# Kernel optimization log

Measured on AMD Instinct MI355X. Metric: run time of the kernel, lower is better.

## Reference

```python
import jax, jax.numpy as jnp
import numpy as np

GROUPS = 32  # from analyze_enhance_linear_ops(4096, 4096, 0.05): smallest divisor g with 1/g <= 0.05


def setup_inputs() -> dict:
    key = jax.random.key(0)
    k1, k2, k3, k4, k5 = jax.random.split(key, 5)
    B, S, D_in, D_out = 4, 2048, 4096, 4096
    ig = D_out // GROUPS  # 128
    x = jax.random.normal(k1, (B, S, D_in), dtype=jnp.float32)
    W = jax.random.normal(k2, (D_out, D_in), dtype=jnp.float32) * 0.02
    b = jax.random.normal(k3, (D_out,), dtype=jnp.float32) * 0.02
    Wg = jax.random.normal(k4, (GROUPS, ig, ig), dtype=jnp.float32) * 0.02
    bg = jax.random.normal(k5, (GROUPS, ig), dtype=jnp.float32) * 0.02
    return {"x": x, "W": W, "b": b, "Wg": Wg, "bg": bg}


def reference(x, W, b, Wg, bg):
    # original_linear: dense GEMM, torch Linear layout W[out, in]
    y = jnp.einsum('bsi,oi->bso', x, W) + b            # [B, S, D_out]
    # GroupedLinear: block-diagonal transform over groups of size out_group
    B, S, D = y.shape
    G, og, ig = Wg.shape
    yg = y.reshape(B, S, G, ig)                        # split into groups
    out = jnp.einsum('bsgi,goi->bsgo', yg, Wg) + bg    # per-group small GEMM + bias
    return out.reshape(B, S, D)                        # cat along feature dim
```

## Files before the change

### kernel.cpp

```cpp
#include <hip/hip_runtime.h>
#include <hip/hip_bf16.h>
#include <stdint.h>

typedef float f32x4 __attribute__((ext_vector_type(4)));
typedef float f32x16 __attribute__((ext_vector_type(16)));
typedef short s16x8 __attribute__((ext_vector_type(8)));
typedef unsigned int u32x2 __attribute__((ext_vector_type(2)));
typedef unsigned int u32x4 __attribute__((ext_vector_type(4)));

#define MDIM 8192
#define NDIM 4096
#define KDIM 4096
#define NKT  64

__device__ __forceinline__ unsigned pkbf(float lo, float hi) {
  unsigned short l = __builtin_bit_cast(unsigned short, __float2bfloat16(lo));
  unsigned short h = __builtin_bit_cast(unsigned short, __float2bfloat16(hi));
  return ((unsigned)h << 16) | (unsigned)l;
}

__device__ __forceinline__ void gload16(const void* g, void* l) {
  __builtin_amdgcn_global_load_lds((const __attribute__((address_space(1))) int*)g,
                                   (__attribute__((address_space(3))) int*)l, 16, 0, 0);
}

__global__ __launch_bounds__(256) void conv_tile(
    const float* __restrict__ X, const float* __restrict__ W,
    s16x8* __restrict__ wsA, s16x8* __restrict__ wsB) {
  __shared__ char lds[32768];
  const int b = blockIdx.x;
  const int tid = threadIdx.x;
  const float* src;
  s16x8* dst;
  int bi;
  if (b < 32 * NKT) { src = X; dst = wsA; bi = b; }
  else              { src = W; dst = wsB; bi = b - 32 * NKT; }
  const int rt = bi >> 6;
  const int kt = bi & 63;
  const int fr = tid >> 4;
  const int c4 = (tid & 15) * 4;
  const int h = c4 >> 5;
  const int ks2 = (c4 >> 4) & 1;
  const int lh = (c4 & 15) >> 3;
  const int e2 = (c4 & 7) * 2;
  #pragma unroll
  for (int f = 0; f < 16; ++f) {
    const int row = f * 16 + fr;
    f32x4 v = *(const f32x4*)(src + ((size_t)rt * 256 + row) * KDIM + kt * 64 + c4);
    u32x2 p = { pkbf(v[0], v[1]), pkbf(v[2], v[3]) };
    const int frag = (h * 2 + ks2) * 8 + (f >> 1);
    const int lane = lh * 32 + (f & 1) * 16 + fr;
    *(u32x2*)(lds + frag * 1024 + lane * 16 + e2) = p;
  }
  __syncthreads();
  const size_t ob = (size_t)bi * 2048;
  #pragma unroll
  for (int i = 0; i < 8; ++i)
    dst[ob + i * 256 + tid] = *(const s16x8*)(lds + (i * 256 + tid) * 16);
}

__global__ __launch_bounds__(512, 2) void gemm256(
    const s16x8* __restrict__ wsA, const s16x8* __restrict__ wsB,
    const float* __restrict__ bias, const float* __restrict__ Wg,
    const float* __restrict__ bg, float* __restrict__ out) {
  extern __shared__ char smem[];
  const int tid = threadIdx.x;
  const int lane = tid & 63;
  const int wid = tid >> 6;
  const int wr = wid >> 2;
  const int wc = wid & 3;
  const int c32 = lane & 31;
  const int q5 = lane >> 5;

  const int bid = blockIdx.x;
  const int swz = (bid & 7) * 64 + (bid >> 3);
  const int bm = swz >> 4;
  const int bn = swz & 15;

  const size_t aBase = (size_t)bm * NKT * 2048;
  const size_t bBase = (size_t)bn * NKT * 2048;

  auto stage = [&](int kt, int db, int isB, int h) {
    const s16x8* s = (isB ? wsB + bBase : wsA + aBase)
                     + (size_t)kt * 2048 + h * 1024 + wid * 128 + lane;
    char* d = smem + isB * 65536 + db * 32768 + h * 16384 + wid * 2048;
    gload16(s, d);
    gload16(s + 64, d + 1024);
  };

  const char* aRd = smem + wr * 4096 + lane * 16;
  const char* bRd = smem + 65536 + wc * 2048 + lane * 16;

  f32x16 acc[4][2];
  #pragma unroll
  for (int m = 0; m < 4; ++m)
    #pragma unroll
    for (int n = 0; n < 2; ++n) acc[m][n] = (f32x16)0.0f;

  s16x8 af[4], bfr[2];

#define SP(DB, H, KS2, SKT, SDB, SOP, SH, DOVM)                                \
  {                                                                            \
    stage(SKT, SDB, SOP, SH);                                                  \
    _Pragma("unroll")                                                          \
    for (int n = 0; n < 2; ++n)                                                \
      bfr[n] = *(const s16x8*)(bRd + (DB)*32768 + (H)*16384 + (KS2)*8192 + n * 1024); \
    _Pragma("unroll")                                                          \
    for (int m = 0; m < 4; ++m)                                                \
      af[m] = *(const s16x8*)(aRd + (DB)*32768 + (H)*16384 + (KS2)*8192 + m * 1024);  \
    if (DOVM) asm volatile("s_waitcnt vmcnt(4)" ::: "memory");                 \
    __builtin_amdgcn_s_barrier();                                              \
    asm volatile("s_waitcnt lgkmcnt(0)" ::: "memory");                         \
    __builtin_amdgcn_s_setprio(1);                                             \
    _Pragma("unroll")                                                          \
    for (int m = 0; m < 4; ++m) {                                              \
      _Pragma("unroll")                                                        \
      for (int n = 0; n < 2; ++n)                                              \
        acc[m][n] = __builtin_amdgcn_mfma_f32_32x32x16_bf16(                   \
            af[m], bfr[n], acc[m][n], 0, 0, 0);                                \
    }                                                                          \
    __builtin_amdgcn_s_setprio(0);                                             \
  }

  stage(0, 0, 0, 0); stage(0, 0, 1, 0);
  stage(0, 0, 0, 1); stage(0, 0, 1, 1);
  stage(1, 1, 0, 0); stage(1, 1, 1, 0);
  asm volatile("s_waitcnt vmcnt(4)" ::: "memory");
  __builtin_amdgcn_s_barrier();

  #pragma clang loop unroll(disable)
  for (int it = 0; it < 32; ++it) {
    const int u0 = 2 * it;
    const int k1 = u0 + 1;
    const int k2 = (u0 + 2 < NKT) ? u0 + 2 : NKT - 1;
    const int k3 = (u0 + 3 < NKT) ? u0 + 3 : NKT - 1;
    SP(0, 0, 0, k1, 1, 0, 1, 0)
    SP(0, 0, 1, k1, 1, 1, 1, 0)
    SP(0, 1, 0, k2, 0, 0, 0, 0)
    SP(0, 1, 1, k2, 0, 1, 0, 1)
    SP(1, 0, 0, k2, 0, 0, 1, 0)
    SP(1, 0, 1, k2, 0, 1, 1, 0)
    SP(1, 1, 0, k3, 1, 0, 0, 0)
    SP(1, 1, 1, k3, 1, 1, 0, 1)
  }
#undef SP

  asm volatile("s_waitcnt vmcnt(0)" ::: "memory");
  asm volatile("s_waitcnt lgkmcnt(0)" ::: "memory");
  __builtin_amdgcn_s_barrier();

  float bv[2];
  #pragma unroll
  for (int n = 0; n < 2; ++n) bv[n] = bias[bn * 256 + wc * 64 + n * 32 + c32];

  {
    const int e2 = (c32 & 7) * 2;
    const int lh = (c32 >> 3) & 1;
    #pragma unroll
    for (int m = 0; m < 4; ++m) {
      const int Mf = wr * 4 + m;
      #pragma unroll
      for (int n = 0; n < 2; ++n) {
        const int Kc = wc * 4 + n * 2 + (c32 >> 4);
        char* base = smem + (Mf * 16 + Kc) * 1024 + lh * 512 + e2;
        #pragma unroll
        for (int r = 0; r < 16; ++r) {
          const int rl = (r & 3) + 8 * (r >> 2) + 4 * q5;
          const float y = acc[m][n][r] + bv[n];
          *(unsigned short*)(base + rl * 16) =
              __builtin_bit_cast(unsigned short, __float2bfloat16(y));
        }
      }
    }
  }
  asm volatile("s_waitcnt lgkmcnt(0)" ::: "memory");
  __builtin_amdgcn_s_barrier();

  const int g = bn * 2 + (wc >> 1);
  const float* wgb = Wg + (size_t)g * 16384;
  f32x16 acc2[4][2];
  #pragma unroll
  for (int m = 0; m < 4; ++m)
    #pragma unroll
    for (int n = 0; n < 2; ++n) acc2[m][n] = (f32x16)0.0f;

  #pragma unroll
  for (int ks = 0; ks < 8; ++ks) {
    const int Kc = (wc >> 1) * 8 + ks;
    s16x8 af2[4];
    #pragma unroll
    for (int m = 0; m < 4; ++m)
      af2[m] = *(const s16x8*)(smem + ((wr * 4 + m) * 16 + Kc) * 1024 + lane * 16);
    #pragma unroll
    for (int n = 0; n < 2; ++n) {
      const int ocl = (wc & 1) * 64 + n * 32 + c32;
      const float* wp = wgb + ocl * 128 + ks * 16 + q5 * 8;
      f32x4 w0 = *(const f32x4*)wp;
      f32x4 w1 = *(const f32x4*)(wp + 4);
      u32x4 pw = { pkbf(w0[0], w0[1]), pkbf(w0[2], w0[3]),
                   pkbf(w1[0], w1[1]), pkbf(w1[2], w1[3]) };
      const s16x8 bfw = __builtin_bit_cast(s16x8, pw);
      #pragma unroll
      for (int m = 0; m < 4; ++m)
        acc2[m][n] = __builtin_amdgcn_mfma_f32_32x32x16_bf16(af2[m], bfw, acc2[m][n], 0, 0, 0);
    }
  }

  float bgv[2];
  #pragma unroll
  for (int n = 0; n < 2; ++n) bgv[n] = bg[bn * 256 + wc * 64 + n * 32 + c32];

  #pragma unroll
  for (int m = 0; m < 4; ++m) {
    #pragma unroll
    for (int n = 0; n < 2; ++n) {
      const int col = bn * 256 + wc * 64 + n * 32 + c32;
      #pragma unroll
      for (int r = 0; r < 16; ++r) {
        const size_t row = (size_t)bm * 256 + wr * 128 + m * 32
                         + (r & 3) + 8 * (r >> 2) + 4 * q5;
        out[row * NDIM + col] = acc2[m][n][r] + bgv[n];
      }
    }
  }
}

extern "C" void kernel_launch(void* const* d_in, const int* in_sizes, int n_in,
                              void* d_out, int out_size, void* d_ws, size_t ws_size,
                              hipStream_t stream) {
  const float* X    = (const float*)d_in[0];
  const float* W    = (const float*)d_in[1];
  const float* bias = (const float*)d_in[2];
  const float* Wg   = (const float*)d_in[3];
  const float* bg   = (const float*)d_in[4];
  float* out = (float*)d_out;

  s16x8* wsA = (s16x8*)d_ws;
  s16x8* wsB = wsA + ((size_t)MDIM * KDIM / 8);

  hipFuncSetAttribute(reinterpret_cast<const void*>(gemm256),
                      hipFuncAttributeMaxDynamicSharedMemorySize, 131072);

  conv_tile<<<dim3(3072), dim3(256), 0, stream>>>(X, W, wsA, wsB);
  gemm256<<<dim3(512), dim3(512), 131072, stream>>>(wsA, wsB, bias, Wg, bg, out);
}
```

Before: 310.3 us.

## Load B fragments directly from global into registers, stage only A in LDS

The B operand is no longer staged through shared memory. Each wave loads its B fragments straight from global memory into registers, double-buffered across k-steps, while A keeps a 4-slot LDS ring. This halves LDS traffic and async-copy bookkeeping, but each B tile is now fetched separately by every wave row instead of once per block. That relies on cache hits, and exposed global latency may stall the MFMAs.

```diff
diff --git a/kernel.cpp b/kernel.cpp
--- a/kernel.cpp
+++ b/kernel.cpp
@@ -77,19 +77,17 @@
   const int bm = swz >> 4;
   const int bn = swz & 15;
 
-  const size_t aBase = (size_t)bm * NKT * 2048;
-  const size_t bBase = (size_t)bn * NKT * 2048;
-
-  auto stage = [&](int kt, int db, int isB, int h) {
-    const s16x8* s = (isB ? wsB + bBase : wsA + aBase)
-                     + (size_t)kt * 2048 + h * 1024 + wid * 128 + lane;
-    char* d = smem + isB * 65536 + db * 32768 + h * 16384 + wid * 2048;
+  const char* wsAb = (const char*)wsA + ((size_t)bm << 21);
+  const char* wsBb = (const char*)wsB + ((size_t)bn << 21);
+
+  auto stageA = [&](int t, int slot) {
+    const char* s = wsAb + ((size_t)t << 14) + (wid << 11) + (lane << 4);
+    char* d = smem + (slot << 14) + (wid << 11);
     gload16(s, d);
-    gload16(s + 64, d + 1024);
+    gload16(s + 1024, d + 1024);
   };
 
-  const char* aRd = smem + wr * 4096 + lane * 16;
-  const char* bRd = smem + 65536 + wc * 2048 + lane * 16;
+  const char* aRd = smem + (wr << 12) + (lane << 4);
 
   f32x16 acc[4][2];
   #pragma unroll
@@ -97,53 +95,58 @@
     #pragma unroll
     for (int n = 0; n < 2; ++n) acc[m][n] = (f32x16)0.0f;
 
-  s16x8 af[4], bfr[2];
-
-#define SP(DB, H, KS2, SKT, SDB, SOP, SH, DOVM)                                \
-  {                                                                            \
-    stage(SKT, SDB, SOP, SH);                                                  \
-    _Pragma("unroll")                                                          \
-    for (int n = 0; n < 2; ++n)                                                \
-      bfr[n] = *(const s16x8*)(bRd + (DB)*32768 + (H)*16384 + (KS2)*8192 + n * 1024); \
-    _Pragma("unroll")                                                          \
-    for (int m = 0; m < 4; ++m)                                                \
-      af[m] = *(const s16x8*)(aRd + (DB)*32768 + (H)*16384 + (KS2)*8192 + m * 1024);  \
-    if (DOVM) asm volatile("s_waitcnt vmcnt(4)" ::: "memory");                 \
-    __builtin_amdgcn_s_barrier();                                              \
-    asm volatile("s_waitcnt lgkmcnt(0)" ::: "memory");                         \
-    __builtin_amdgcn_s_setprio(1);                                             \
-    _Pragma("unroll")                                                          \
-    for (int m = 0; m < 4; ++m) {                                              \
-      _Pragma("unroll")                                                        \
-      for (int n = 0; n < 2; ++n)                                              \
-        acc[m][n] = __builtin_amdgcn_mfma_f32_32x32x16_bf16(                   \
-            af[m], bfr[n], acc[m][n], 0, 0, 0);                                \
-    }                                                                          \
-    __builtin_amdgcn_s_setprio(0);                                             \
-  }
-
-  stage(0, 0, 0, 0); stage(0, 0, 1, 0);
-  stage(0, 0, 0, 1); stage(0, 0, 1, 1);
-  stage(1, 1, 0, 0); stage(1, 1, 1, 0);
-  asm volatile("s_waitcnt vmcnt(4)" ::: "memory");
+  s16x8 af[4], bE[2], bO[2];
+
+  const char* bAddr = wsBb + ((wc * 2) << 10) + (lane << 4);
+
+  stageA(0, 0);
+  stageA(1, 1);
+  #pragma unroll
+  for (int n = 0; n < 2; ++n)
+    bE[n] = *(const s16x8*)(bAddr + ((size_t)0 << 13) + (n << 10));
+  asm volatile("s_waitcnt vmcnt(2)" ::: "memory");
   __builtin_amdgcn_s_barrier();
 
   #pragma clang loop unroll(disable)
-  for (int it = 0; it < 32; ++it) {
-    const int u0 = 2 * it;
-    const int k1 = u0 + 1;
-    const int k2 = (u0 + 2 < NKT) ? u0 + 2 : NKT - 1;
-    const int k3 = (u0 + 3 < NKT) ? u0 + 3 : NKT - 1;
-    SP(0, 0, 0, k1, 1, 0, 1, 0)
-    SP(0, 0, 1, k1, 1, 1, 1, 0)
-    SP(0, 1, 0, k2, 0, 0, 0, 0)
-    SP(0, 1, 1, k2, 0, 1, 0, 1)
-    SP(1, 0, 0, k2, 0, 0, 1, 0)
-    SP(1, 0, 1, k2, 0, 1, 1, 0)
-    SP(1, 1, 0, k3, 1, 0, 0, 0)
-    SP(1, 1, 1, k3, 1, 1, 0, 1)
-  }
-#undef SP
+  for (int t = 0; t < 128; ++t) {
+    const int tn = (t + 2 < 128) ? t + 2 : 127;
+    const size_t k1 = 2 * t + 1;
+    const size_t k2 = (2 * t + 2 < 256) ? 2 * t + 2 : 255;
+    const int slot = t & 3;
+    stageA(tn, (t + 2) & 3);
+    #pragma unroll
+    for (int n = 0; n < 2; ++n)
+      bO[n] = *(const s16x8*)(bAddr + (k1 << 13) + (n << 10));
+    #pragma unroll
+    for (int m = 0; m < 4; ++m)
+      af[m] = *(const s16x8*)(aRd + (slot << 14) + (m << 10));
+    asm volatile("s_waitcnt vmcnt(4)" ::: "memory");
+    __builtin_amdgcn_s_barrier();
+    __builtin_amdgcn_s_setprio(1);
+    #pragma unroll
+    for (int m = 0; m < 4; ++m) {
+      #pragma unroll
+      for (int n = 0; n < 2; ++n)
+        acc[m][n] = __builtin_amdgcn_mfma_f32_32x32x16_bf16(af[m], bE[n], acc[m][n], 0, 0, 0);
+    }
+    __builtin_amdgcn_s_setprio(0);
+    #pragma unroll
+    for (int n = 0; n < 2; ++n)
+      bE[n] = *(const s16x8*)(bAddr + (k2 << 13) + (n << 10));
+    #pragma unroll
+    for (int m = 0; m < 4; ++m)
+      af[m] = *(const s16x8*)(aRd + (slot << 14) + 8192 + (m << 10));
+    asm volatile("s_waitcnt vmcnt(4)" ::: "memory");
+    __builtin_amdgcn_s_barrier();
+    __builtin_amdgcn_s_setprio(1);
+    #pragma unroll
+    for (int m = 0; m < 4; ++m) {
+      #pragma unroll
+      for (int n = 0; n < 2; ++n)
+        acc[m][n] = __builtin_amdgcn_mfma_f32_32x32x16_bf16(af[m], bO[n], acc[m][n], 0, 0, 0);
+    }
+    __builtin_amdgcn_s_setprio(0);
+  }
 
   asm volatile("s_waitcnt vmcnt(0)" ::: "memory");
   asm volatile("s_waitcnt lgkmcnt(0)" ::: "memory");
```

New measurement: 340.5 us. 9.7% more time.
